# Performance work log

Hardware: AMD Instinct MI355X
Metric: run time of the kernel (lower is better)

## Reference

```python
import jax, jax.numpy as jnp
import numpy as np

DIM = 64
SQRT_DIM = float(np.sqrt(DIM))


def setup_inputs() -> dict:
    key = jax.random.key(0)
    k1, k2, k3, k4 = jax.random.split(key, 4)
    B, S, D = 32, 2048, DIM
    query = jax.random.normal(k1, (B, S, D), dtype=jnp.float32)
    key_t = jax.random.normal(k2, (B, S, D), dtype=jnp.float32)
    value = jax.random.normal(k3, (B, S, D), dtype=jnp.float32)
    mask = jax.random.randint(k4, (B, S, S), 0, 2).astype(jnp.bool_)
    return {"query": query, "key": key_t, "value": value, "mask": mask}


def reference(query, key, value, mask):
    # score: [B, S, S]
    score = jnp.einsum('bqd,bkd->bqk', query, key) / SQRT_DIM
    score = jnp.where(mask, -jnp.inf, score)
    attn = jax.nn.softmax(score, axis=-1)
    # fully-masked rows produce NaN in softmax; torch.nan_to_num -> 0
    attn = jnp.nan_to_num(attn, nan=0.0)
    context = jnp.einsum('bqk,bkd->bqd', attn, value)
    return context
```

## Files before the change

### kernel.cpp

```cpp
#include <hip/hip_runtime.h>
#include <hip/hip_bf16.h>

#define BATCH 32
#define SEQ   2048
#define DIM   64
#define KT    64
#define NIT   (SEQ / KT)
#define QTB   256

typedef __attribute__((ext_vector_type(8))) short bf16x8;
typedef __attribute__((ext_vector_type(4))) short bf16x4;
typedef __attribute__((ext_vector_type(4))) float fx4;
typedef __attribute__((ext_vector_type(4))) int   ix4;

static __device__ __forceinline__ short f2bf(float f) {
    __bf16 h = (__bf16)f;
    return *(short*)&h;
}
static __device__ __forceinline__ bf16x4 cvt4(float a, float b, float c, float d) {
    bf16x4 s; s[0] = f2bf(a); s[1] = f2bf(b); s[2] = f2bf(c); s[3] = f2bf(d);
    return s;
}

#define QSCALE (0.125f * 1.44269504088896f)

__global__ __launch_bounds__(1024, 4)
void attn_fwd(const float* __restrict__ Qg, const float* __restrict__ Kg,
              const float* __restrict__ Vg, const int* __restrict__ Mg,
              float* __restrict__ Og)
{
    __shared__ __align__(16) char smem[32768];

    const int bid   = (int)((blockIdx.x & 7) * 32 + (blockIdx.x >> 3));
    const int b     = bid >> 3;
    const int qbase = (bid & 7) * QTB;
    const int tid   = threadIdx.x;
    const int wave  = tid >> 6;
    const int lane  = tid & 63;
    const int l15   = lane & 15;
    const int g     = lane >> 4;

    const int qrow_g = qbase + wave * 16 + l15;
    const float* qrow = Qg + ((size_t)(b * SEQ + qrow_g) * DIM);
    bf16x8 qf[2];
#pragma unroll
    for (int h = 0; h < 2; ++h) {
        fx4 a = *(const fx4*)(qrow + h * 32 + g * 8);
        fx4 c = *(const fx4*)(qrow + h * 32 + g * 8 + 4);
        a *= QSCALE; c *= QSCALE;
        bf16x8 q;
        q[0]=f2bf(a[0]); q[1]=f2bf(a[1]); q[2]=f2bf(a[2]); q[3]=f2bf(a[3]);
        q[4]=f2bf(c[0]); q[5]=f2bf(c[1]); q[6]=f2bf(c[2]); q[7]=f2bf(c[3]);
        qf[h] = q;
    }

    const int rg = lane >> 4, cq = lane & 15;
    const int* mload = Mg + ((size_t)(b * SEQ + qbase + wave * 16 + rg) * SEQ) + cq * 4;

    const bool srb0 = (l15 & 4) != 0;
    const bool srb1 = (l15 & 8) != 0;
    const int  mbase = (l15 & 3) * 16 + g;

    const int kr = tid >> 4, kcq = tid & 15;
    const float* ksrc = Kg + ((size_t)(b * SEQ + kr) * DIM) + kcq * 4;
    const int kwofs = kr * 128 + ((kcq * 8) ^ ((kr & 7) * 16));

    const int vd = tid & 63, jg = tid >> 6;
    const float* vsrc = Vg + ((size_t)(b * SEQ + jg * 4) * DIM) + vd;
    const int vpr = vd >> 1, vu = vd & 1, jg7 = jg & 7;
    const int vwofs = 16384 + (jg >> 3) * 4096 + vpr * 128 +
                      (((vu * 64) + 16 * (jg7 & 3) + 8 * (jg7 >> 2)) ^ ((vpr & 7) * 16));

    const int ksw  = (l15 & 7) * 16;
    const int koh0 = l15 * 128 + ((16 * g)      ^ ksw);
    const int koh1 = l15 * 128 + ((16 * g + 64) ^ ksw);
    const int vrof = (l15 >> 1) * 128 + (((l15 & 1) * 64 + 16 * g) ^ ((l15 >> 1) * 16));

    fx4 acc[4] = {};
    float lsum = 0.f;

    fx4   kReg[2];
    float vReg[2][4];
    ix4   m[4];

    {
        fx4 k0 = *(const fx4*)(ksrc);
        float v0[4];
#pragma unroll
        for (int i = 0; i < 4; ++i) v0[i] = vsrc[(size_t)i * DIM];
        kReg[0] = *(const fx4*)(ksrc + (size_t)KT * DIM);
#pragma unroll
        for (int i = 0; i < 4; ++i) vReg[0][i] = vsrc[(size_t)(KT + i) * DIM];
#pragma unroll
        for (int s = 0; s < 4; ++s)
            m[s] = __builtin_nontemporal_load((const ix4*)(mload + (size_t)4 * s * SEQ));
        *(bf16x4*)(smem + kwofs) = cvt4(k0[0], k0[1], k0[2], k0[3]);
        *(bf16x4*)(smem + vwofs) = cvt4(v0[0], v0[1], v0[2], v0[3]);
    }
    asm volatile("s_waitcnt lgkmcnt(0)" ::: "memory");
    __builtin_amdgcn_s_barrier();
    __builtin_amdgcn_sched_barrier(0);

#pragma unroll 2
    for (int kt = 0; kt < NIT; ++kt) {
        const int cur = kt & 1, nxt = cur ^ 1;
        const int kb2 = ((kt + 2) & (NIT - 1)) * KT;
        const int kb1 = ((kt + 1) & (NIT - 1)) * KT;

        kReg[nxt] = *(const fx4*)(ksrc + (size_t)kb2 * DIM);
#pragma unroll
        for (int i = 0; i < 4; ++i) vReg[nxt][i] = vsrc[(size_t)(kb2 + i) * DIM];

        const char* kB = smem + cur * 8192;
        fx4 sc[4];
#pragma unroll
        for (int s = 0; s < 4; ++s) {
            bf16x8 kf0 = *(const bf16x8*)(kB + s * 2048 + koh0);
            bf16x8 kf1 = *(const bf16x8*)(kB + s * 2048 + koh1);
            fx4 t = {};
            t = __builtin_amdgcn_mfma_f32_16x16x32_bf16(kf0, qf[0], t, 0, 0, 0);
            t = __builtin_amdgcn_mfma_f32_16x16x32_bf16(kf1, qf[1], t, 0, 0, 0);
            sc[s] = t;
        }

        unsigned long long bal[4][4];
#pragma unroll
        for (int s = 0; s < 4; ++s)
#pragma unroll
            for (int i = 0; i < 4; ++i)
                bal[s][i] = __ballot(m[s][i] != 0);

#pragma unroll
        for (int s = 0; s < 4; ++s)
            m[s] = __builtin_nontemporal_load((const ix4*)(mload + (size_t)4 * s * SEQ + kb1));

        float p[16];
#pragma unroll
        for (int i = 0; i < 4; ++i) {
            unsigned long long W = srb1 ? (srb0 ? bal[3][i] : bal[2][i])
                                        : (srb0 ? bal[1][i] : bal[0][i]);
            unsigned bits = (unsigned)(W >> mbase);
            p[0 + i]  = (bits & 1u)         ? 0.f : __builtin_amdgcn_exp2f(sc[0][i]);
            p[4 + i]  = ((bits >> 4) & 1u)  ? 0.f : __builtin_amdgcn_exp2f(sc[1][i]);
            p[8 + i]  = ((bits >> 8) & 1u)  ? 0.f : __builtin_amdgcn_exp2f(sc[2][i]);
            p[12 + i] = ((bits >> 12) & 1u) ? 0.f : __builtin_amdgcn_exp2f(sc[3][i]);
        }

        lsum += (((p[0] + p[1]) + (p[2] + p[3])) + ((p[4] + p[5]) + (p[6] + p[7])))
              + (((p[8] + p[9]) + (p[10] + p[11])) + ((p[12] + p[13]) + (p[14] + p[15])));

        bf16x8 pf0, pf1;
#pragma unroll
        for (int j = 0; j < 8; ++j) { pf0[j] = f2bf(p[j]); pf1[j] = f2bf(p[8 + j]); }

        const char* vB = smem + 16384 + cur * 8192 + vrof;
#pragma unroll
        for (int dsub = 0; dsub < 4; ++dsub) {
            bf16x8 vf = *(const bf16x8*)(vB + dsub * 1024);
            acc[dsub] = __builtin_amdgcn_mfma_f32_16x16x32_bf16(vf, pf0, acc[dsub], 0, 0, 0);
        }
#pragma unroll
        for (int dsub = 0; dsub < 4; ++dsub) {
            bf16x8 vf = *(const bf16x8*)(vB + 4096 + dsub * 1024);
            acc[dsub] = __builtin_amdgcn_mfma_f32_16x16x32_bf16(vf, pf1, acc[dsub], 0, 0, 0);
        }

        *(bf16x4*)(smem + nxt * 8192 + kwofs) =
            cvt4(kReg[cur][0], kReg[cur][1], kReg[cur][2], kReg[cur][3]);
        *(bf16x4*)(smem + nxt * 8192 + vwofs) =
            cvt4(vReg[cur][0], vReg[cur][1], vReg[cur][2], vReg[cur][3]);

        asm volatile("s_waitcnt lgkmcnt(0)" ::: "memory");
        __builtin_amdgcn_s_barrier();
        __builtin_amdgcn_sched_barrier(0);
    }

    lsum += __shfl_xor(lsum, 16);
    lsum += __shfl_xor(lsum, 32);
    const float inv = lsum > 0.f ? 1.0f / lsum : 0.f;

    float* obase = Og + ((size_t)(b * SEQ + qrow_g) * DIM) + 4 * g;
#pragma unroll
    for (int dsub = 0; dsub < 4; ++dsub) {
        fx4 o = acc[dsub] * inv;
        __builtin_nontemporal_store(o, (fx4*)(obase + dsub * 16));
    }
}

extern "C" void kernel_launch(void* const* d_in, const int* in_sizes, int n_in,
                              void* d_out, int out_size, void* d_ws, size_t ws_size,
                              hipStream_t stream) {
    const float* Q = (const float*)d_in[0];
    const float* K = (const float*)d_in[1];
    const float* V = (const float*)d_in[2];
    const int*   M = (const int*)d_in[3];
    float*       O = (float*)d_out;
    dim3 grid(BATCH * (SEQ / QTB));
    attn_fwd<<<grid, 1024, 0, stream>>>(Q, K, V, M, O);
}
```

Measured before the change: 124.0 us.

## Halve query tile per block to 512 threads with wider K/V staging loads

```diff
diff --git a/kernel.cpp b/kernel.cpp
--- a/kernel.cpp
+++ b/kernel.cpp
@@ -6,7 +6,7 @@
 #define DIM   64
 #define KT    64
 #define NIT   (SEQ / KT)
-#define QTB   256
+#define QTB   128
 
 typedef __attribute__((ext_vector_type(8))) short bf16x8;
 typedef __attribute__((ext_vector_type(4))) short bf16x4;
@@ -17,6 +17,12 @@
     __bf16 h = (__bf16)f;
     return *(short*)&h;
 }
+static __device__ __forceinline__ bf16x8 cvt8(fx4 a, fx4 b) {
+    bf16x8 s;
+    s[0] = f2bf(a[0]); s[1] = f2bf(a[1]); s[2] = f2bf(a[2]); s[3] = f2bf(a[3]);
+    s[4] = f2bf(b[0]); s[5] = f2bf(b[1]); s[6] = f2bf(b[2]); s[7] = f2bf(b[3]);
+    return s;
+}
 static __device__ __forceinline__ bf16x4 cvt4(float a, float b, float c, float d) {
     bf16x4 s; s[0] = f2bf(a); s[1] = f2bf(b); s[2] = f2bf(c); s[3] = f2bf(d);
     return s;
@@ -24,16 +30,16 @@
 
 #define QSCALE (0.125f * 1.44269504088896f)
 
-__global__ __launch_bounds__(1024, 4)
+__global__ __launch_bounds__(512, 4)
 void attn_fwd(const float* __restrict__ Qg, const float* __restrict__ Kg,
               const float* __restrict__ Vg, const int* __restrict__ Mg,
               float* __restrict__ Og)
 {
     __shared__ __align__(16) char smem[32768];
 
-    const int bid   = (int)((blockIdx.x & 7) * 32 + (blockIdx.x >> 3));
-    const int b     = bid >> 3;
-    const int qbase = (bid & 7) * QTB;
+    const int bid   = (int)((blockIdx.x & 7) * 64 + (blockIdx.x >> 3));
+    const int b     = bid >> 4;
+    const int qbase = (bid & 15) * QTB;
     const int tid   = threadIdx.x;
     const int wave  = tid >> 6;
     const int lane  = tid & 63;
@@ -48,10 +54,7 @@
         fx4 a = *(const fx4*)(qrow + h * 32 + g * 8);
         fx4 c = *(const fx4*)(qrow + h * 32 + g * 8 + 4);
         a *= QSCALE; c *= QSCALE;
-        bf16x8 q;
-        q[0]=f2bf(a[0]); q[1]=f2bf(a[1]); q[2]=f2bf(a[2]); q[3]=f2bf(a[3]);
-        q[4]=f2bf(c[0]); q[5]=f2bf(c[1]); q[6]=f2bf(c[2]); q[7]=f2bf(c[3]);
-        qf[h] = q;
+        qf[h] = cvt8(a, c);
     }
 
     const int rg = lane >> 4, cq = lane & 15;
@@ -61,15 +64,18 @@
     const bool srb1 = (l15 & 8) != 0;
     const int  mbase = (l15 & 3) * 16 + g;
 
-    const int kr = tid >> 4, kcq = tid & 15;
-    const float* ksrc = Kg + ((size_t)(b * SEQ + kr) * DIM) + kcq * 4;
-    const int kwofs = kr * 128 + ((kcq * 8) ^ ((kr & 7) * 16));
-
-    const int vd = tid & 63, jg = tid >> 6;
-    const float* vsrc = Vg + ((size_t)(b * SEQ + jg * 4) * DIM) + vd;
-    const int vpr = vd >> 1, vu = vd & 1, jg7 = jg & 7;
-    const int vwofs = 16384 + (jg >> 3) * 4096 + vpr * 128 +
-                      (((vu * 64) + 16 * (jg7 & 3) + 8 * (jg7 >> 2)) ^ ((vpr & 7) * 16));
+    const int kr = tid >> 3, kc8 = tid & 7;
+    const float* ksrc = Kg + ((size_t)(b * SEQ + kr) * DIM) + kc8 * 8;
+    const int kwofs = kr * 128 + ((kc8 * 16) ^ ((kr & 7) * 16));
+
+    const int vd = tid & 63, jg8 = tid >> 6;
+    const float* vsrc = Vg + ((size_t)(b * SEQ + jg8 * 8) * DIM) + vd;
+    const int vpr = vd >> 1, vu = vd & 1, q3 = jg8 & 3, vh = jg8 >> 2;
+    const int vsw = (vpr & 7) * 16;
+    const int vwofs0 = 16384 + vh * 4096 + vpr * 128 +
+                       (((vu * 64) + 16 * ((2 * q3) & 3)     + 8 * (q3 >> 1)) ^ vsw);
+    const int vwofs1 = 16384 + vh * 4096 + vpr * 128 +
+                       (((vu * 64) + 16 * ((2 * q3 + 1) & 3) + 8 * (q3 >> 1)) ^ vsw);
 
     const int ksw  = (l15 & 7) * 16;
     const int koh0 = l15 * 128 + ((16 * g)      ^ ksw);
@@ -79,23 +85,26 @@
     fx4 acc[4] = {};
     float lsum = 0.f;
 
-    fx4   kReg[2];
-    float vReg[2][4];
+    fx4   kReg[2][2];
+    float vReg[2][8];
     ix4   m[4];
 
     {
-        fx4 k0 = *(const fx4*)(ksrc);
-        float v0[4];
-#pragma unroll
-        for (int i = 0; i < 4; ++i) v0[i] = vsrc[(size_t)i * DIM];
-        kReg[0] = *(const fx4*)(ksrc + (size_t)KT * DIM);
-#pragma unroll
-        for (int i = 0; i < 4; ++i) vReg[0][i] = vsrc[(size_t)(KT + i) * DIM];
+        fx4 kA = *(const fx4*)(ksrc);
+        fx4 kB = *(const fx4*)(ksrc + 4);
+        float v0[8];
+#pragma unroll
+        for (int i = 0; i < 8; ++i) v0[i] = vsrc[(size_t)i * DIM];
+        kReg[0][0] = *(const fx4*)(ksrc + (size_t)KT * DIM);
+        kReg[0][1] = *(const fx4*)(ksrc + (size_t)KT * DIM + 4);
+#pragma unroll
+        for (int i = 0; i < 8; ++i) vReg[0][i] = vsrc[(size_t)(KT + i) * DIM];
 #pragma unroll
         for (int s = 0; s < 4; ++s)
             m[s] = __builtin_nontemporal_load((const ix4*)(mload + (size_t)4 * s * SEQ));
-        *(bf16x4*)(smem + kwofs) = cvt4(k0[0], k0[1], k0[2], k0[3]);
-        *(bf16x4*)(smem + vwofs) = cvt4(v0[0], v0[1], v0[2], v0[3]);
+        *(bf16x8*)(smem + kwofs) = cvt8(kA, kB);
+        *(bf16x4*)(smem + vwofs0) = cvt4(v0[0], v0[1], v0[2], v0[3]);
+        *(bf16x4*)(smem + vwofs1) = cvt4(v0[4], v0[5], v0[6], v0[7]);
     }
     asm volatile("s_waitcnt lgkmcnt(0)" ::: "memory");
     __builtin_amdgcn_s_barrier();
@@ -107,16 +116,17 @@
         const int kb2 = ((kt + 2) & (NIT - 1)) * KT;
         const int kb1 = ((kt + 1) & (NIT - 1)) * KT;
 
-        kReg[nxt] = *(const fx4*)(ksrc + (size_t)kb2 * DIM);
-#pragma unroll
-        for (int i = 0; i < 4; ++i) vReg[nxt][i] = vsrc[(size_t)(kb2 + i) * DIM];
-
-        const char* kB = smem + cur * 8192;
+        kReg[nxt][0] = *(const fx4*)(ksrc + (size_t)kb2 * DIM);
+        kReg[nxt][1] = *(const fx4*)(ksrc + (size_t)kb2 * DIM + 4);
+#pragma unroll
+        for (int i = 0; i < 8; ++i) vReg[nxt][i] = vsrc[(size_t)(kb2 + i) * DIM];
+
+        const char* kB_ = smem + cur * 8192;
         fx4 sc[4];
 #pragma unroll
         for (int s = 0; s < 4; ++s) {
-            bf16x8 kf0 = *(const bf16x8*)(kB + s * 2048 + koh0);
-            bf16x8 kf1 = *(const bf16x8*)(kB + s * 2048 + koh1);
+            bf16x8 kf0 = *(const bf16x8*)(kB_ + s * 2048 + koh0);
+            bf16x8 kf1 = *(const bf16x8*)(kB_ + s * 2048 + koh1);
             fx4 t = {};
             t = __builtin_amdgcn_mfma_f32_16x16x32_bf16(kf0, qf[0], t, 0, 0, 0);
             t = __builtin_amdgcn_mfma_f32_16x16x32_bf16(kf1, qf[1], t, 0, 0, 0);
@@ -153,22 +163,23 @@
 #pragma unroll
         for (int j = 0; j < 8; ++j) { pf0[j] = f2bf(p[j]); pf1[j] = f2bf(p[8 + j]); }
 
-        const char* vB = smem + 16384 + cur * 8192 + vrof;
+        const char* vB_ = smem + 16384 + cur * 8192 + vrof;
 #pragma unroll
         for (int dsub = 0; dsub < 4; ++dsub) {
-            bf16x8 vf = *(const bf16x8*)(vB + dsub * 1024);
+            bf16x8 vf = *(const bf16x8*)(vB_ + dsub * 1024);
             acc[dsub] = __builtin_amdgcn_mfma_f32_16x16x32_bf16(vf, pf0, acc[dsub], 0, 0, 0);
         }
 #pragma unroll
         for (int dsub = 0; dsub < 4; ++dsub) {
-            bf16x8 vf = *(const bf16x8*)(vB + 4096 + dsub * 1024);
+            bf16x8 vf = *(const bf16x8*)(vB_ + 4096 + dsub * 1024);
             acc[dsub] = __builtin_amdgcn_mfma_f32_16x16x32_bf16(vf, pf1, acc[dsub], 0, 0, 0);
         }
 
-        *(bf16x4*)(smem + nxt * 8192 + kwofs) =
-            cvt4(kReg[cur][0], kReg[cur][1], kReg[cur][2], kReg[cur][3]);
-        *(bf16x4*)(smem + nxt * 8192 + vwofs) =
+        *(bf16x8*)(smem + nxt * 8192 + kwofs) = cvt8(kReg[cur][0], kReg[cur][1]);
+        *(bf16x4*)(smem + nxt * 8192 + vwofs0) =
             cvt4(vReg[cur][0], vReg[cur][1], vReg[cur][2], vReg[cur][3]);
+        *(bf16x4*)(smem + nxt * 8192 + vwofs1) =
+            cvt4(vReg[cur][4], vReg[cur][5], vReg[cur][6], vReg[cur][7]);
 
         asm volatile("s_waitcnt lgkmcnt(0)" ::: "memory");
         __builtin_amdgcn_s_barrier();
@@ -196,5 +207,5 @@
     const int*   M = (const int*)d_in[3];
     float*       O = (float*)d_out;
     dim3 grid(BATCH * (SEQ / QTB));
-    attn_fwd<<<grid, 1024, 0, stream>>>(Q, K, V, M, O);
-}
+    attn_fwd<<<grid, 512, 0, stream>>>(Q, K, V, M, O);
+}
```

Measured after the change: 118.9 us, median of 2. -4.1%, faster.
